# Kernel optimization log

Hardware: AMD Instinct MI355X
Metric: run time of the kernel (lower is better)

Reference implementation:

```python
import jax, jax.numpy as jnp
import numpy as np

HEADS = 2
BN_EPS = 1e-5


def _upsample2x_bilinear_ac(x):
    # torch nn.Upsample(scale_factor=2, mode='bilinear', align_corners=True)
    B, C, H, W = x.shape

    def grid(n):
        c = jnp.arange(2 * n) * ((n - 1) / (2 * n - 1))  # align_corners mapping
        i0 = jnp.clip(jnp.floor(c).astype(jnp.int32), 0, n - 2)
        w = (c - i0).astype(x.dtype)
        return i0, w

    i0, wh = grid(H)
    j0, ww = grid(W)
    x = x[:, :, i0, :] * (1 - wh)[None, None, :, None] + x[:, :, i0 + 1, :] * wh[None, None, :, None]
    x = x[:, :, :, j0] * (1 - ww) + x[:, :, :, j0 + 1] * ww
    return x


def _self_attn(x, wq, wkv, wo, wob):
    # x: (b, t, d); lucidrains axial_attention SelfAttention
    b, t, d = x.shape
    e = d // HEADS
    q = x @ wq
    k, v = jnp.split(x @ wkv, 2, axis=-1)
    mh = lambda z: z.reshape(b, t, HEADS, e).transpose(0, 2, 1, 3)  # (b,h,t,e)
    q, k, v = mh(q), mh(k), mh(v)
    dots = jnp.einsum('bhie,bhje->bhij', q, k) * (e ** -0.5)
    attn = jax.nn.softmax(dots, axis=-1)
    o = jnp.einsum('bhij,bhje->bhie', attn, v)
    o = o.transpose(0, 2, 1, 3).reshape(b, t, d)
    return o @ wo + wob


def setup_inputs() -> dict:
    key = jax.random.key(0)
    ks = jax.random.split(key, 16)
    C, E = 256, 128
    cat = 2 * C + E
    s = 0.02
    inp = {
        'x': jax.random.normal(ks[0], (4, C, 64, 64), jnp.float32),
        'res': jax.random.normal(ks[1], (4, E, 128, 128), jnp.float32),
        'wq_h': jax.random.normal(ks[2], (C, C), jnp.float32) * s,
        'wkv_h': jax.random.normal(ks[3], (C, 2 * C), jnp.float32) * s,
        'wo_h': jax.random.normal(ks[4], (C, C), jnp.float32) * s,
        'wob_h': jnp.zeros((C,), jnp.float32),
        'wq_w': jax.random.normal(ks[5], (C, C), jnp.float32) * s,
        'wkv_w': jax.random.normal(ks[6], (C, 2 * C), jnp.float32) * s,
        'wo_w': jax.random.normal(ks[7], (C, C), jnp.float32) * s,
        'wob_w': jnp.zeros((C,), jnp.float32),
        'conv_w': jax.random.normal(ks[8], (cat, E), jnp.float32) * s,
        'gamma': jnp.ones((E,), jnp.float32),
        'beta': jnp.zeros((E,), jnp.float32),
    }
    return inp


def reference(x, res, wq_h, wkv_h, wo_h, wob_h, wq_w, wkv_w, wo_w, wob_w, conv_w, gamma, beta):
    xu = _upsample2x_bilinear_ac(x)  # (B,C,2H,2W)
    B, C, H, W = xu.shape
    # axial attention along H (rows): batch over B*W
    ah = xu.transpose(0, 3, 2, 1).reshape(B * W, H, C)
    ah = _self_attn(ah, wq_h, wkv_h, wo_h, wob_h).reshape(B, W, H, C).transpose(0, 3, 2, 1)
    # axial attention along W (cols): batch over B*H
    aw = xu.transpose(0, 2, 3, 1).reshape(B * H, W, C)
    aw = _self_attn(aw, wq_w, wkv_w, wo_w, wob_w).reshape(B, H, W, C).transpose(0, 3, 1, 2)
    x_attn = jax.nn.relu(ah + aw)  # sum_axial_out=True, then ReLU
    cat = jnp.concatenate([x_attn, xu, res], axis=1)  # (B, 2C+E, H, W)
    y = jnp.einsum('bchw,ce->behw', cat, conv_w)  # conv1x1, no bias
    y = jax.nn.relu(y)
    # BatchNorm2d, training-mode batch stats (biased variance)
    mu = y.mean(axis=(0, 2, 3), keepdims=True)
    var = y.var(axis=(0, 2, 3), keepdims=True)
    y = (y - mu) / jnp.sqrt(var + BN_EPS)
    return y * gamma[None, :, None, None] + beta[None, :, None, None]
```

## Files before the change

kernel.cpp:

```cpp
#include <hip/hip_runtime.h>
#include <hip/hip_bf16.h>
#include <cstdio>


typedef short bf16x8 __attribute__((ext_vector_type(8)));
typedef short bf16x4 __attribute__((ext_vector_type(4)));
typedef float f32x4 __attribute__((ext_vector_type(4)));

#define MFMA16(a, b, c) __builtin_amdgcn_mfma_f32_16x16x32_bf16((a), (b), (c), 0, 0, 0)

__device__ __forceinline__ short f2bf(float v) {
  __hip_bfloat16 h = __float2bfloat16(v);
  union { __hip_bfloat16 h; short s; } u; u.h = h; return u.s;
}
__device__ __forceinline__ float bf2f(short s) {
  return __uint_as_float(((unsigned int)(unsigned short)s) << 16);
}
__device__ __forceinline__ int swz(int row, int col) {
  return col ^ ((row & 7) << 3);
}

struct WtAll {
  const float* src[7];
  short* dst[7];
  int K[7], N[7], tile0[7];
};

__global__ __launch_bounds__(256) void k_wt_all(WtAll P) {
  const int bid = blockIdx.x;
  int i = 0;
#pragma unroll
  for (int j = 1; j < 7; j++) if (bid >= P.tile0[j]) i = j;
  const float* src = P.src[i];
  short* dst = P.dst[i];
  const int K = P.K[i], N = P.N[i];
  const int local = bid - P.tile0[i];
  const int ktiles = K >> 5;
  const int nt = local / ktiles, kt = local - nt * ktiles;
  const int k0 = kt * 32, n0 = nt * 32;
  __shared__ float tile[32][33];
  const int tx = threadIdx.x & 31, ty = threadIdx.x >> 5;
#pragma unroll
  for (int r = 0; r < 4; r++)
    tile[ty + r * 8][tx] = src[(size_t)(k0 + ty + r * 8) * N + n0 + tx];
  __syncthreads();
#pragma unroll
  for (int r = 0; r < 4; r++)
    dst[(size_t)(n0 + ty + r * 8) * K + k0 + tx] = f2bf(tile[tx][ty + r * 8]);
}

__global__ __launch_bounds__(256) void k_upsample(const float* __restrict__ x,
                                                  short* __restrict__ xu) {
  __shared__ float ldsV[64][65];
  const int bh = blockIdx.x, z = blockIdx.y;
  const int b = bh >> 7, h = bh & 127;
  const float chf = h * (63.0f / 127.0f);
  int i0 = (int)chf; if (i0 > 62) i0 = 62;
  const float wh = chf - (float)i0;
  const int t = threadIdx.x;
  const int cbase = z * 64;
  const float* xb = x + ((size_t)(b * 256 + cbase) * 64 + i0) * 64;
#pragma unroll
  for (int p = 0; p < 16; p++) {
    const int li = p * 256 + t;
    const int c = li >> 6, w = li & 63;
    const float* px = xb + (size_t)c * 4096 + w;
    const float v0 = px[0], v1 = px[64];
    ldsV[c][w] = v0 * (1.f - wh) + v1 * wh;
  }
  __syncthreads();
  const int cg = t & 7, wi = t >> 3;
  short* xout = xu + (size_t)(bh * 128) * 256 + cbase + cg * 8;
#pragma unroll
  for (int p = 0; p < 4; p++) {
    const int w = p * 32 + wi;
    const float cwf = w * (63.0f / 127.0f);
    int j0 = (int)cwf; if (j0 > 62) j0 = 62;
    const float ww = cwf - (float)j0;
    bf16x8 o;
#pragma unroll
    for (int u = 0; u < 8; u++) {
      const float v0 = ldsV[cg * 8 + u][j0], v1 = ldsV[cg * 8 + u][j0 + 1];
      o[u] = f2bf(v0 * (1.f - ww) + v1 * ww);
    }
    *(bf16x8*)(xout + (size_t)w * 256) = o;
  }
}

__global__ __launch_bounds__(512, 2) void k_fused(const short* __restrict__ xu,
                                                  const short* __restrict__ wqkvT,
                                                  const short* __restrict__ woT,
                                                  const float* __restrict__ wob,
                                                  short* __restrict__ accb,
                                                  int dir) {
  __shared__ __align__(16) short Xs[128][256];
  __shared__ __align__(16) short Qb[128][128];
  __shared__ __align__(16) short Kb[128][128];
  __shared__ __align__(16) short Vtb[128][128];

  const int s = blockIdx.x;
  const int b = s >> 7, pos = s & 127;
  const int tok0 = b * 16384 + (dir ? pos * 128 : pos);
  const int tstep = dir ? 1 : 128;
  const int tid = threadIdx.x;
  const int lane = tid & 63, wid = tid >> 6;
  const int lr = lane & 15, kb = lane >> 4;
  const int ct = wid * 16;
  const float scale = 0.08838834764831845f;

#pragma unroll
  for (int p = 0; p < 8; p++) {
    const int u = p * 512 + tid;
    const int row = u >> 5, ck = (u & 31) * 8;
    bf16x8 v = *(const bf16x8*)(xu + (size_t)(tok0 + row * tstep) * 256 + ck);
    *(bf16x8*)&Xs[row][swz(row, ck)] = v;
  }

  f32x4 accp[2][8];
#pragma unroll
  for (int i = 0; i < 2; i++)
#pragma unroll
    for (int j = 0; j < 8; j++) accp[i][j] = (f32x4){0.f, 0.f, 0.f, 0.f};

  for (int h = 0; h < 2; h++) {
    __syncthreads();

    {
      const short* wqb = wqkvT + (size_t)(h * 128 + ct + lr) * 256 + kb * 8;
      const short* wkb = wqkvT + (size_t)(256 + h * 128 + ct + lr) * 256 + kb * 8;
      bf16x8 wq[8], wk[8];
#pragma unroll
      for (int ks = 0; ks < 8; ks++) {
        wq[ks] = *(const bf16x8*)(wqb + ks * 32);
        wk[ks] = *(const bf16x8*)(wkb + ks * 32);
      }
#pragma unroll
      for (int nt = 0; nt < 8; nt++) {
        const int xrow = nt * 16 + lr;
        f32x4 dq = (f32x4){0.f, 0.f, 0.f, 0.f};
        f32x4 dk = (f32x4){0.f, 0.f, 0.f, 0.f};
#pragma unroll
        for (int ks = 0; ks < 8; ks++) {
          bf16x8 xf = *(const bf16x8*)&Xs[xrow][swz(xrow, kb * 8 + ks * 32)];
          dq = MFMA16(wq[ks], xf, dq);
          dk = MFMA16(wk[ks], xf, dk);
        }
        const int trow = nt * 16 + lr, cc = ct + kb * 4;
        bf16x4 pq = {f2bf(dq[0]), f2bf(dq[1]), f2bf(dq[2]), f2bf(dq[3])};
        bf16x4 pk = {f2bf(dk[0]), f2bf(dk[1]), f2bf(dk[2]), f2bf(dk[3])};
        *(bf16x4*)&Qb[trow][swz(trow, cc)] = pq;
        *(bf16x4*)&Kb[trow][swz(trow, cc)] = pk;
      }
    }
    {
      const short* wvb = wqkvT + (size_t)(512 + h * 128 + ct + lr) * 256 + kb * 8;
      bf16x8 wv[8];
#pragma unroll
      for (int ks = 0; ks < 8; ks++) wv[ks] = *(const bf16x8*)(wvb + ks * 32);
#pragma unroll
      for (int nt = 0; nt < 8; nt++) {
        const int xrow = nt * 16 + lr;
        f32x4 dv = (f32x4){0.f, 0.f, 0.f, 0.f};
#pragma unroll
        for (int ks = 0; ks < 8; ks++) {
          bf16x8 xf = *(const bf16x8*)&Xs[xrow][swz(xrow, kb * 8 + ks * 32)];
          dv = MFMA16(wv[ks], xf, dv);
        }
        const int col = nt * 16 + lr;
#pragma unroll
        for (int r = 0; r < 4; r++) {
          const int vrow = ct + kb * 4 + r;
          Vtb[vrow][swz(vrow, col)] = f2bf(dv[r]);
        }
      }
    }

    __syncthreads();

    f32x4 s8[8];
#pragma unroll
    for (int i = 0; i < 8; i++) s8[i] = (f32x4){0.f, 0.f, 0.f, 0.f};
    const int qrow = ct + lr;
#pragma unroll
    for (int ks = 0; ks < 4; ks++) {
      bf16x8 aq = *(const bf16x8*)&Qb[qrow][swz(qrow, kb * 8 + ks * 32)];
#pragma unroll
      for (int nj = 0; nj < 8; nj++) {
        const int krow = nj * 16 + lr;
        bf16x8 bk = *(const bf16x8*)&Kb[krow][swz(krow, kb * 8 + ks * 32)];
        s8[nj] = MFMA16(aq, bk, s8[nj]);
      }
    }
#pragma unroll
    for (int rr = 0; rr < 4; rr++) {
      float m = s8[0][rr];
#pragma unroll
      for (int nj = 1; nj < 8; nj++) m = fmaxf(m, s8[nj][rr]);
      m = fmaxf(m, __shfl_xor(m, 1)); m = fmaxf(m, __shfl_xor(m, 2));
      m = fmaxf(m, __shfl_xor(m, 4)); m = fmaxf(m, __shfl_xor(m, 8));
      float p[8], sum = 0.f;
#pragma unroll
      for (int nj = 0; nj < 8; nj++) { p[nj] = __expf((s8[nj][rr] - m) * scale); sum += p[nj]; }
      sum += __shfl_xor(sum, 1); sum += __shfl_xor(sum, 2);
      sum += __shfl_xor(sum, 4); sum += __shfl_xor(sum, 8);
      const float inv = 1.f / sum;
      const int prow = ct + kb * 4 + rr;
#pragma unroll
      for (int nj = 0; nj < 8; nj++)
        Qb[prow][swz(prow, nj * 16 + lr)] = f2bf(p[nj] * inv);
    }

    __syncthreads();

    f32x4 o8[8];
#pragma unroll
    for (int i = 0; i < 8; i++) o8[i] = (f32x4){0.f, 0.f, 0.f, 0.f};
#pragma unroll
    for (int ks = 0; ks < 4; ks++) {
      bf16x8 bp = *(const bf16x8*)&Qb[qrow][swz(qrow, kb * 8 + ks * 32)];
#pragma unroll
      for (int mi = 0; mi < 8; mi++) {
        const int vrow = mi * 16 + lr;
        bf16x8 av = *(const bf16x8*)&Vtb[vrow][swz(vrow, kb * 8 + ks * 32)];
        o8[mi] = MFMA16(av, bp, o8[mi]);
      }
    }
    const int orow = ct + lr;
#pragma unroll
    for (int mi = 0; mi < 8; mi++) {
      const int cc = mi * 16 + kb * 4;
      bf16x4 po = {f2bf(o8[mi][0]), f2bf(o8[mi][1]), f2bf(o8[mi][2]), f2bf(o8[mi][3])};
      *(bf16x4*)&Kb[orow][swz(orow, cc)] = po;
    }

    __syncthreads();

    {
      const short* w0 = woT + (size_t)(wid * 32 + lr) * 256 + h * 128 + kb * 8;
      const short* w1 = woT + (size_t)(wid * 32 + 16 + lr) * 256 + h * 128 + kb * 8;
      bf16x8 wa[4], wb[4];
#pragma unroll
      for (int ks = 0; ks < 4; ks++) {
        wa[ks] = *(const bf16x8*)(w0 + ks * 32);
        wb[ks] = *(const bf16x8*)(w1 + ks * 32);
      }
#pragma unroll
      for (int nt = 0; nt < 8; nt++) {
        const int trow = nt * 16 + lr;
#pragma unroll
        for (int ks = 0; ks < 4; ks++) {
          bf16x8 bo = *(const bf16x8*)&Kb[trow][swz(trow, kb * 8 + ks * 32)];
          accp[0][nt] = MFMA16(wa[ks], bo, accp[0][nt]);
          accp[1][nt] = MFMA16(wb[ks], bo, accp[1][nt]);
        }
      }
    }
  }

#pragma unroll
  for (int mi2 = 0; mi2 < 2; mi2++) {
    const int outc = wid * 32 + mi2 * 16 + kb * 4;
    const float b0 = wob[outc], b1 = wob[outc + 1];
    const float b2 = wob[outc + 2], b3 = wob[outc + 3];
#pragma unroll
    for (int nt = 0; nt < 8; nt++) {
      const int token = tok0 + (nt * 16 + lr) * tstep;
      short* op = accb + (size_t)token * 256 + outc;
      float v0 = accp[mi2][nt][0] + b0, v1 = accp[mi2][nt][1] + b1;
      float v2 = accp[mi2][nt][2] + b2, v3 = accp[mi2][nt][3] + b3;
      if (dir) {
        bf16x4 old = *(const bf16x4*)op;
        v0 += bf2f(old[0]); v1 += bf2f(old[1]);
        v2 += bf2f(old[2]); v3 += bf2f(old[3]);
      }
      bf16x4 pv = {f2bf(v0), f2bf(v1), f2bf(v2), f2bf(v3)};
      *(bf16x4*)op = pv;
    }
  }
}

__global__ __launch_bounds__(256) void k_gemm_conv(const short* __restrict__ accb,
                                                   const short* __restrict__ xu,
                                                   const float* __restrict__ res,
                                                   const short* __restrict__ Bt,
                                                   float* __restrict__ ytmp) {
  const int tid = threadIdx.x;
  const int lane = tid & 63, wid = tid >> 6;
  const int lr = lane & 15, kb = lane >> 4;
  const int wr = wid >> 1, wc = wid & 1;
  const int m0 = blockIdx.y * 128;
  f32x4 acc[4][4];
#pragma unroll
  for (int i = 0; i < 4; i++)
#pragma unroll
    for (int j = 0; j < 4; j++) acc[i][j] = (f32x4){0.f, 0.f, 0.f, 0.f};
  const short* arow1 = accb + (size_t)(m0 + wr * 64 + lr) * 256 + kb * 8;
  const short* arow2 = xu + (size_t)(m0 + wr * 64 + lr) * 256 + kb * 8;
  const short* brow = Bt + (size_t)(wc * 64 + lr) * 640 + kb * 8;
#pragma unroll
  for (int ks = 0; ks < 8; ks++) {
    bf16x8 a[4], b[4];
#pragma unroll
    for (int mi = 0; mi < 4; mi++) {
      bf16x8 tv = *(const bf16x8*)(arow1 + (size_t)mi * 16 * 256 + ks * 32);
#pragma unroll
      for (int u = 0; u < 8; u++)
        tv[u] = ((unsigned short)tv[u] & 0x8000u) ? (short)0 : tv[u];
      a[mi] = tv;
    }
#pragma unroll
    for (int nj = 0; nj < 4; nj++)
      b[nj] = *(const bf16x8*)(brow + (size_t)nj * 16 * 640 + ks * 32);
#pragma unroll
    for (int mi = 0; mi < 4; mi++)
#pragma unroll
      for (int nj = 0; nj < 4; nj++)
        acc[mi][nj] = MFMA16(a[mi], b[nj], acc[mi][nj]);
  }
#pragma unroll
  for (int ks = 8; ks < 16; ks++) {
    bf16x8 a[4], b[4];
#pragma unroll
    for (int mi = 0; mi < 4; mi++)
      a[mi] = *(const bf16x8*)(arow2 + (size_t)mi * 16 * 256 + (ks - 8) * 32);
#pragma unroll
    for (int nj = 0; nj < 4; nj++)
      b[nj] = *(const bf16x8*)(brow + (size_t)nj * 16 * 640 + ks * 32);
#pragma unroll
    for (int mi = 0; mi < 4; mi++)
#pragma unroll
      for (int nj = 0; nj < 4; nj++)
        acc[mi][nj] = MFMA16(a[mi], b[nj], acc[mi][nj]);
  }
  const int bC = (m0 >> 14) * 128;
  const int hh = (m0 >> 7) & 127;
#pragma unroll
  for (int ks = 16; ks < 20; ks++) {
    const int e0 = (ks - 16) * 32 + kb * 8;
    bf16x8 a[4], b[4];
#pragma unroll
    for (int mi = 0; mi < 4; mi++) {
      const int wl = wr * 64 + mi * 16 + lr;
      const float* rp = res + ((size_t)(bC + e0) * 128 + hh) * 128 + wl;
      bf16x8 tv;
#pragma unroll
      for (int u = 0; u < 8; u++) tv[u] = f2bf(rp[(size_t)u * 16384]);
      a[mi] = tv;
    }
#pragma unroll
    for (int nj = 0; nj < 4; nj++)
      b[nj] = *(const bf16x8*)(brow + (size_t)nj * 16 * 640 + ks * 32);
#pragma unroll
    for (int mi = 0; mi < 4; mi++)
#pragma unroll
      for (int nj = 0; nj < 4; nj++)
        acc[mi][nj] = MFMA16(a[mi], b[nj], acc[mi][nj]);
  }
#pragma unroll
  for (int mi = 0; mi < 4; mi++) {
    const int rbase = m0 + wr * 64 + mi * 16 + kb * 4;
#pragma unroll
    for (int nj = 0; nj < 4; nj++) {
      const int c = wc * 64 + nj * 16 + lr;
#pragma unroll
      for (int r = 0; r < 4; r++)
        ytmp[(size_t)(rbase + r) * 128 + c] = fmaxf(acc[mi][nj][r], 0.f);
    }
  }
}

__global__ __launch_bounds__(256) void k_bnstats1(const float* __restrict__ y,
                                                  float* __restrict__ partial) {
  const int blk = blockIdx.x, tid = threadIdx.x;
  const int ch = tid & 127, sub = tid >> 7;
  float s = 0.f, s2 = 0.f;
  const float* p = y + (size_t)(blk * 512 + sub) * 128 + ch;
  for (int i = 0; i < 256; i++) {
    float v = p[(size_t)i * 256];
    s += v; s2 += v * v;
  }
  __shared__ float rs[2][128], rs2[2][128];
  rs[sub][ch] = s; rs2[sub][ch] = s2;
  __syncthreads();
  if (tid < 128) {
    partial[(size_t)(blk * 128 + tid) * 2]     = rs[0][tid] + rs[1][tid];
    partial[(size_t)(blk * 128 + tid) * 2 + 1] = rs2[0][tid] + rs2[1][tid];
  }
}

__global__ __launch_bounds__(128) void k_bnstats2(const float* __restrict__ partial,
                                                  float* __restrict__ stats) {
  const int ch = threadIdx.x;
  float s = 0.f, s2 = 0.f;
  for (int i = 0; i < 128; i++) {
    s  += partial[(size_t)(i * 128 + ch) * 2];
    s2 += partial[(size_t)(i * 128 + ch) * 2 + 1];
  }
  const float mu = s * (1.f / 65536.f);
  const float var = s2 * (1.f / 65536.f) - mu * mu;
  stats[ch * 2] = mu;
  stats[ch * 2 + 1] = rsqrtf(var + 1e-5f);
}

__global__ __launch_bounds__(256) void k_bnout(const float* __restrict__ y,
                                               const float* __restrict__ stats,
                                               const float* __restrict__ gamma,
                                               const float* __restrict__ beta,
                                               float* __restrict__ out) {
  const int bh = blockIdx.x;
  const int b = bh >> 7, h = bh & 127;
  const int w = threadIdx.x & 127, eh = threadIdx.x >> 7;
  const float* yp = y + (size_t)(bh * 128 + w) * 128;
  for (int e2 = 0; e2 < 64; e2++) {
    const int e = e2 * 2 + eh;
    const float mu = stats[e * 2], rstd = stats[e * 2 + 1];
    const float v = yp[e];
    out[((size_t)(b * 128 + e) << 14) + h * 128 + w] =
        (v - mu) * rstd * gamma[e] + beta[e];
  }
}

extern "C" void kernel_launch(void* const* d_in, const int* in_sizes, int n_in,
                              void* d_out, int out_size, void* d_ws, size_t ws_size,
                              hipStream_t stream) {
  const float* x      = (const float*)d_in[0];
  const float* res    = (const float*)d_in[1];
  const float* wq_h   = (const float*)d_in[2];
  const float* wkv_h  = (const float*)d_in[3];
  const float* wo_h   = (const float*)d_in[4];
  const float* wob_h  = (const float*)d_in[5];
  const float* wq_w   = (const float*)d_in[6];
  const float* wkv_w  = (const float*)d_in[7];
  const float* wo_w   = (const float*)d_in[8];
  const float* wob_w  = (const float*)d_in[9];
  const float* conv_w = (const float*)d_in[10];
  const float* gamma  = (const float*)d_in[11];
  const float* beta   = (const float*)d_in[12];

  char* ws = (char*)d_ws;
  short* wqkvT[2] = {(short*)(ws + 0), (short*)(ws + 393216)};
  short* woT[2]   = {(short*)(ws + 786432), (short*)(ws + 917504)};
  short* convT    = (short*)(ws + 1048576);
  short* xu       = (short*)(ws + 1245184);
  float* ytmp     = (float*)(ws + 34799616);
  float* partial  = (float*)(ws + 68354048);
  float* stats    = (float*)(ws + 68485120);
  short* accb     = (short*)d_out;
  float* out      = (float*)d_out;

  if (ws_size < 68486144ull)
    fprintf(stderr, "kernel_launch: ws_size %zu too small\n", ws_size);

  WtAll P;
  P.src[0] = wq_h;  P.dst[0] = wqkvT[0];          P.K[0] = 256; P.N[0] = 256; P.tile0[0] = 0;
  P.src[1] = wkv_h; P.dst[1] = wqkvT[0] + 65536;  P.K[1] = 256; P.N[1] = 512; P.tile0[1] = 64;
  P.src[2] = wq_w;  P.dst[2] = wqkvT[1];          P.K[2] = 256; P.N[2] = 256; P.tile0[2] = 192;
  P.src[3] = wkv_w; P.dst[3] = wqkvT[1] + 65536;  P.K[3] = 256; P.N[3] = 512; P.tile0[3] = 256;
  P.src[4] = wo_h;  P.dst[4] = woT[0];            P.K[4] = 256; P.N[4] = 256; P.tile0[4] = 384;
  P.src[5] = wo_w;  P.dst[5] = woT[1];            P.K[5] = 256; P.N[5] = 256; P.tile0[5] = 448;
  P.src[6] = conv_w;P.dst[6] = convT;             P.K[6] = 640; P.N[6] = 128; P.tile0[6] = 512;
  k_wt_all<<<592, 256, 0, stream>>>(P);

  k_upsample<<<dim3(512, 4), 256, 0, stream>>>(x, xu);

  k_fused<<<512, 512, 0, stream>>>(xu, wqkvT[0], woT[0], wob_h, accb, 0);
  k_fused<<<512, 512, 0, stream>>>(xu, wqkvT[1], woT[1], wob_w, accb, 1);

  k_gemm_conv<<<dim3(1, 512), 256, 0, stream>>>(accb, xu, res, convT, ytmp);
  k_bnstats1<<<128, 256, 0, stream>>>(ytmp, partial);
  k_bnstats2<<<1, 128, 0, stream>>>(partial, stats);
  k_bnout<<<512, 256, 0, stream>>>(ytmp, stats, gamma, beta, out);
}
```

Baseline: 270.8 us.

## Fuse QKV projection loops and transpose score MFMA to drop softmax barrier

```diff
diff --git a/kernel.cpp b/kernel.cpp
--- a/kernel.cpp
+++ b/kernel.cpp
@@ -123,56 +123,40 @@
     for (int j = 0; j < 8; j++) accp[i][j] = (f32x4){0.f, 0.f, 0.f, 0.f};
 
   for (int h = 0; h < 2; h++) {
+    const short* wqb = wqkvT + (size_t)(h * 128 + ct + lr) * 256 + kb * 8;
+    const short* wkb = wqkvT + (size_t)(256 + h * 128 + ct + lr) * 256 + kb * 8;
+    const short* wvb = wqkvT + (size_t)(512 + h * 128 + ct + lr) * 256 + kb * 8;
+    bf16x8 wq[8], wk[8], wv[8];
+#pragma unroll
+    for (int ks = 0; ks < 8; ks++) {
+      wq[ks] = *(const bf16x8*)(wqb + ks * 32);
+      wk[ks] = *(const bf16x8*)(wkb + ks * 32);
+      wv[ks] = *(const bf16x8*)(wvb + ks * 32);
+    }
+
     __syncthreads();
 
-    {
-      const short* wqb = wqkvT + (size_t)(h * 128 + ct + lr) * 256 + kb * 8;
-      const short* wkb = wqkvT + (size_t)(256 + h * 128 + ct + lr) * 256 + kb * 8;
-      bf16x8 wq[8], wk[8];
+#pragma unroll
+    for (int nt = 0; nt < 8; nt++) {
+      const int xrow = nt * 16 + lr;
+      f32x4 dq = (f32x4){0.f, 0.f, 0.f, 0.f};
+      f32x4 dk = (f32x4){0.f, 0.f, 0.f, 0.f};
+      f32x4 dv = (f32x4){0.f, 0.f, 0.f, 0.f};
 #pragma unroll
       for (int ks = 0; ks < 8; ks++) {
-        wq[ks] = *(const bf16x8*)(wqb + ks * 32);
-        wk[ks] = *(const bf16x8*)(wkb + ks * 32);
-      }
-#pragma unroll
-      for (int nt = 0; nt < 8; nt++) {
-        const int xrow = nt * 16 + lr;
-        f32x4 dq = (f32x4){0.f, 0.f, 0.f, 0.f};
-        f32x4 dk = (f32x4){0.f, 0.f, 0.f, 0.f};
-#pragma unroll
-        for (int ks = 0; ks < 8; ks++) {
-          bf16x8 xf = *(const bf16x8*)&Xs[xrow][swz(xrow, kb * 8 + ks * 32)];
-          dq = MFMA16(wq[ks], xf, dq);
-          dk = MFMA16(wk[ks], xf, dk);
-        }
-        const int trow = nt * 16 + lr, cc = ct + kb * 4;
-        bf16x4 pq = {f2bf(dq[0]), f2bf(dq[1]), f2bf(dq[2]), f2bf(dq[3])};
-        bf16x4 pk = {f2bf(dk[0]), f2bf(dk[1]), f2bf(dk[2]), f2bf(dk[3])};
-        *(bf16x4*)&Qb[trow][swz(trow, cc)] = pq;
-        *(bf16x4*)&Kb[trow][swz(trow, cc)] = pk;
-      }
-    }
-    {
-      const short* wvb = wqkvT + (size_t)(512 + h * 128 + ct + lr) * 256 + kb * 8;
-      bf16x8 wv[8];
-#pragma unroll
-      for (int ks = 0; ks < 8; ks++) wv[ks] = *(const bf16x8*)(wvb + ks * 32);
-#pragma unroll
-      for (int nt = 0; nt < 8; nt++) {
-        const int xrow = nt * 16 + lr;
-        f32x4 dv = (f32x4){0.f, 0.f, 0.f, 0.f};
-#pragma unroll
-        for (int ks = 0; ks < 8; ks++) {
-          bf16x8 xf = *(const bf16x8*)&Xs[xrow][swz(xrow, kb * 8 + ks * 32)];
-          dv = MFMA16(wv[ks], xf, dv);
-        }
-        const int col = nt * 16 + lr;
-#pragma unroll
-        for (int r = 0; r < 4; r++) {
-          const int vrow = ct + kb * 4 + r;
-          Vtb[vrow][swz(vrow, col)] = f2bf(dv[r]);
-        }
-      }
+        bf16x8 xf = *(const bf16x8*)&Xs[xrow][swz(xrow, kb * 8 + ks * 32)];
+        dq = MFMA16(wq[ks], xf, dq);
+        dk = MFMA16(wk[ks], xf, dk);
+        dv = MFMA16(xf, wv[ks], dv);
+      }
+      const int trow = nt * 16 + lr, cc = ct + kb * 4;
+      bf16x4 pq = {f2bf(dq[0]), f2bf(dq[1]), f2bf(dq[2]), f2bf(dq[3])};
+      bf16x4 pk = {f2bf(dk[0]), f2bf(dk[1]), f2bf(dk[2]), f2bf(dk[3])};
+      *(bf16x4*)&Qb[trow][swz(trow, cc)] = pq;
+      *(bf16x4*)&Kb[trow][swz(trow, cc)] = pk;
+      const int vrow = ct + lr;
+      bf16x4 pv = {f2bf(dv[0]), f2bf(dv[1]), f2bf(dv[2]), f2bf(dv[3])};
+      *(bf16x4*)&Vtb[vrow][swz(vrow, nt * 16 + kb * 4)] = pv;
     }
 
     __syncthreads();
@@ -188,29 +172,35 @@
       for (int nj = 0; nj < 8; nj++) {
         const int krow = nj * 16 + lr;
         bf16x8 bk = *(const bf16x8*)&Kb[krow][swz(krow, kb * 8 + ks * 32)];
-        s8[nj] = MFMA16(aq, bk, s8[nj]);
-      }
-    }
-#pragma unroll
-    for (int rr = 0; rr < 4; rr++) {
-      float m = s8[0][rr];
-#pragma unroll
-      for (int nj = 1; nj < 8; nj++) m = fmaxf(m, s8[nj][rr]);
-      m = fmaxf(m, __shfl_xor(m, 1)); m = fmaxf(m, __shfl_xor(m, 2));
-      m = fmaxf(m, __shfl_xor(m, 4)); m = fmaxf(m, __shfl_xor(m, 8));
-      float p[8], sum = 0.f;
-#pragma unroll
-      for (int nj = 0; nj < 8; nj++) { p[nj] = __expf((s8[nj][rr] - m) * scale); sum += p[nj]; }
-      sum += __shfl_xor(sum, 1); sum += __shfl_xor(sum, 2);
-      sum += __shfl_xor(sum, 4); sum += __shfl_xor(sum, 8);
+        s8[nj] = MFMA16(bk, aq, s8[nj]);
+      }
+    }
+    {
+      float m = s8[0][0];
+#pragma unroll
+      for (int nj = 0; nj < 8; nj++)
+#pragma unroll
+        for (int r = 0; r < 4; r++) m = fmaxf(m, s8[nj][r]);
+      m = fmaxf(m, __shfl_xor(m, 16));
+      m = fmaxf(m, __shfl_xor(m, 32));
+      float sum = 0.f;
+#pragma unroll
+      for (int nj = 0; nj < 8; nj++)
+#pragma unroll
+        for (int r = 0; r < 4; r++) {
+          s8[nj][r] = __expf((s8[nj][r] - m) * scale);
+          sum += s8[nj][r];
+        }
+      sum += __shfl_xor(sum, 16);
+      sum += __shfl_xor(sum, 32);
       const float inv = 1.f / sum;
-      const int prow = ct + kb * 4 + rr;
-#pragma unroll
-      for (int nj = 0; nj < 8; nj++)
-        Qb[prow][swz(prow, nj * 16 + lr)] = f2bf(p[nj] * inv);
-    }
-
-    __syncthreads();
+#pragma unroll
+      for (int nj = 0; nj < 8; nj++) {
+        bf16x4 pp = {f2bf(s8[nj][0] * inv), f2bf(s8[nj][1] * inv),
+                     f2bf(s8[nj][2] * inv), f2bf(s8[nj][3] * inv)};
+        *(bf16x4*)&Qb[qrow][swz(qrow, nj * 16 + kb * 4)] = pp;
+      }
+    }
 
     f32x4 o8[8];
 #pragma unroll
@@ -225,12 +215,14 @@
         o8[mi] = MFMA16(av, bp, o8[mi]);
       }
     }
-    const int orow = ct + lr;
+
+    __syncthreads();
+
 #pragma unroll
     for (int mi = 0; mi < 8; mi++) {
       const int cc = mi * 16 + kb * 4;
       bf16x4 po = {f2bf(o8[mi][0]), f2bf(o8[mi][1]), f2bf(o8[mi][2]), f2bf(o8[mi][3])};
-      *(bf16x4*)&Kb[orow][swz(orow, cc)] = po;
+      *(bf16x4*)&Kb[qrow][swz(qrow, cc)] = po;
     }
 
     __syncthreads();
@@ -238,11 +230,11 @@
     {
       const short* w0 = woT + (size_t)(wid * 32 + lr) * 256 + h * 128 + kb * 8;
       const short* w1 = woT + (size_t)(wid * 32 + 16 + lr) * 256 + h * 128 + kb * 8;
-      bf16x8 wa[4], wb[4];
+      bf16x8 wa[4], wb2[4];
 #pragma unroll
       for (int ks = 0; ks < 4; ks++) {
-        wa[ks] = *(const bf16x8*)(w0 + ks * 32);
-        wb[ks] = *(const bf16x8*)(w1 + ks * 32);
+        wa[ks]  = *(const bf16x8*)(w0 + ks * 32);
+        wb2[ks] = *(const bf16x8*)(w1 + ks * 32);
       }
 #pragma unroll
       for (int nt = 0; nt < 8; nt++) {
@@ -251,7 +243,7 @@
         for (int ks = 0; ks < 4; ks++) {
           bf16x8 bo = *(const bf16x8*)&Kb[trow][swz(trow, kb * 8 + ks * 32)];
           accp[0][nt] = MFMA16(wa[ks], bo, accp[0][nt]);
-          accp[1][nt] = MFMA16(wb[ks], bo, accp[1][nt]);
+          accp[1][nt] = MFMA16(wb2[ks], bo, accp[1][nt]);
         }
       }
     }
```

New measurement: 253.6 us. 1.07x faster.
